# Kernel tuning notes

Hardware: AMD Instinct MI355X
Metric: run time of the kernel (lower is better)

Reference implementation:

```python
import jax, jax.numpy as jnp
import numpy as np

N_NODES = 100000
N_EDGES = 1600000
IN_CH, HID_CH, OUT_CH = 128, 256, 128


def _sage_conv(x, src, dst, W_l, b_l, W_r, n_nodes):
    """PyG SAGEConv with mean aggregation: lin_l(mean_j x_j) + lin_r(x)."""
    # gather source features per edge, scatter-sum into destination nodes
    agg = jax.ops.segment_sum(x[src], dst, num_segments=n_nodes)  # [N, C]
    deg = jax.ops.segment_sum(jnp.ones((src.shape[0],), x.dtype), dst,
                              num_segments=n_nodes)               # [N]
    mean = agg / jnp.maximum(deg, 1.0)[:, None]
    return mean @ W_l + b_l + x @ W_r


def setup_inputs() -> dict:
    key = jax.random.key(0)
    ks = jax.random.split(key, 8)
    x = jax.random.normal(ks[0], (N_NODES, IN_CH), dtype=jnp.float32)
    edge_index = jax.random.randint(ks[1], (2, N_EDGES), 0, N_NODES, dtype=jnp.int64)
    s1 = 1.0 / np.sqrt(IN_CH)
    s2 = 1.0 / np.sqrt(HID_CH)
    W1_l = jax.random.normal(ks[2], (IN_CH, HID_CH), dtype=jnp.float32) * s1
    W1_r = jax.random.normal(ks[3], (IN_CH, HID_CH), dtype=jnp.float32) * s1
    b1 = jnp.zeros((HID_CH,), dtype=jnp.float32)
    W2_l = jax.random.normal(ks[4], (HID_CH, OUT_CH), dtype=jnp.float32) * s2
    W2_r = jax.random.normal(ks[5], (HID_CH, OUT_CH), dtype=jnp.float32) * s2
    b2 = jnp.zeros((OUT_CH,), dtype=jnp.float32)
    return {"x": x, "edge_index": edge_index, "W1_l": W1_l, "b1": b1,
            "W1_r": W1_r, "W2_l": W2_l, "b2": b2, "W2_r": W2_r}


def reference(x, edge_index, W1_l, b1, W1_r, W2_l, b2, W2_r):
    src, dst = edge_index[0], edge_index[1]
    h = _sage_conv(x, src, dst, W1_l, b1, W1_r, N_NODES)
    h = jax.nn.relu(h)
    out = _sage_conv(h, src, dst, W2_l, b2, W2_r, N_NODES)
    return out
```

## Files before the change

kernel.cpp:

```cpp
#include <hip/hip_runtime.h>
#include <cstddef>

#define N_NODES_C 100000
#define N_EDGES_C 1600000

#define NPB 126
#define NB 794
#define DIV_MAGIC 34087043ULL
#define BCAP 2560

#define CONV_BLOCKS 12500
#define WB_BLOCKS 512
#define P1_BLOCKS 1563

typedef unsigned short u16;
typedef __attribute__((ext_vector_type(8))) short bf16x8;
typedef __attribute__((ext_vector_type(4))) float f32x4;

__device__ __forceinline__ u16 f2bf(float f) {
    unsigned u = __float_as_uint(f);
    u += 0x7fffu + ((u >> 16) & 1);
    return (u16)(u >> 16);
}
__device__ __forceinline__ float bf2f(u16 b) {
    return __uint_as_float(((unsigned)b) << 16);
}
__device__ __forceinline__ unsigned bucket_of(int d) {
    return (unsigned)(((unsigned long long)(unsigned)d * DIV_MAGIC) >> 32);
}


__global__ __launch_bounds__(256) void front_fused(
    const float* __restrict__ x, const int* __restrict__ dst,
    const float* __restrict__ W1l, const float* __restrict__ W1r,
    const float* __restrict__ W2l, const float* __restrict__ W2r,
    u16* __restrict__ x_bf, u16* __restrict__ T1l, u16* __restrict__ T1r,
    u16* __restrict__ T2l, u16* __restrict__ T2r,
    int* __restrict__ bucket_counts) {
    const int b = blockIdx.x;
    const int t = threadIdx.x;
    if (b < CONV_BLOCKS) {
        int i = b * 256 + t;
        if (i < 3200000) {
            float4 v = ((const float4*)x)[i];
            ushort4 o;
            o.x = f2bf(v.x); o.y = f2bf(v.y); o.z = f2bf(v.z); o.w = f2bf(v.w);
            ((ushort4*)x_bf)[i] = o;
        }
    } else if (b < CONV_BLOCKS + WB_BLOCKS) {
        int id = (b - CONV_BLOCKS) * 256 + t;
        int which = id >> 15;
        int r = id & 32767;
        if (which == 0) {
            int n = r >> 7, k = r & 127;
            T1l[r] = f2bf(W1l[k * 256 + n]);
        } else if (which == 1) {
            int n = r >> 7, k = r & 127;
            T1r[r] = f2bf(W1r[k * 256 + n]);
        } else if (which == 2) {
            int n = r >> 8, k = r & 255;
            T2l[r] = f2bf(W2l[k * 128 + n]);
        } else {
            int n = r >> 8, k = r & 255;
            T2r[r] = f2bf(W2r[k * 128 + n]);
        }
    } else {
        __shared__ int hist[NB];
        for (int j = t; j < NB; j += 256) hist[j] = 0;
        __syncthreads();
        int i = (b - CONV_BLOCKS - WB_BLOCKS) * 256 + t;
        if (i * 4 < N_EDGES_C) {
            int4 d = ((const int4*)dst)[i];
            atomicAdd(&hist[bucket_of(d.x)], 1);
            atomicAdd(&hist[bucket_of(d.y)], 1);
            atomicAdd(&hist[bucket_of(d.z)], 1);
            atomicAdd(&hist[bucket_of(d.w)], 1);
        }
        __syncthreads();
        for (int j = t; j < NB; j += 256) {
            int c = hist[j];
            if (c) atomicAdd(&bucket_counts[j], c);
        }
    }
}


__global__ __launch_bounds__(1024) void bucket_scan(const int* __restrict__ counts,
                                                    int* __restrict__ base,
                                                    int* __restrict__ cursor) {
    __shared__ int s[1024];
    int t = threadIdx.x;
    int v = (t < NB) ? counts[t] : 0;
    s[t] = v;
    __syncthreads();
    for (int off = 1; off < 1024; off <<= 1) {
        int u = (t >= off) ? s[t - off] : 0;
        __syncthreads();
        s[t] += u;
        __syncthreads();
    }
    if (t < NB) {
        int excl = s[t] - v;
        base[t] = excl;
        cursor[t] = excl;
    }
    if (t == NB - 1) base[NB] = s[t];
}


__global__ __launch_bounds__(1024) void p2_scatter(const int* __restrict__ src,
                                                   const int* __restrict__ dst,
                                                   int* __restrict__ cursor,
                                                   unsigned* __restrict__ edge_pkt) {
    __shared__ int hist[NB];
    __shared__ int lbase[NB];
    __shared__ int cur2[NB];
    int t = threadIdx.x;
    if (t < NB) { hist[t] = 0; cur2[t] = 0; }
    __syncthreads();

    int4 dd[4];
    int idx[4];
#pragma unroll
    for (int r = 0; r < 4; ++r) {
        int i = blockIdx.x * 4096 + r * 1024 + t;
        idx[r] = i;
        if (i * 4 < N_EDGES_C) {
            int4 d = ((const int4*)dst)[i];
            dd[r] = d;
            atomicAdd(&hist[bucket_of(d.x)], 1);
            atomicAdd(&hist[bucket_of(d.y)], 1);
            atomicAdd(&hist[bucket_of(d.z)], 1);
            atomicAdd(&hist[bucket_of(d.w)], 1);
        }
    }
    __syncthreads();
    if (t < NB) {
        int c = hist[t];
        if (c) lbase[t] = atomicAdd(&cursor[t], c);
    }
    __syncthreads();

#pragma unroll
    for (int r = 0; r < 4; ++r) {
        int i = idx[r];
        if (i * 4 < N_EDGES_C) {
            int4 s4 = ((const int4*)src)[i];
            int4 d = dd[r];
            {
                unsigned b = bucket_of(d.x);
                int local = d.x - (int)b * NPB;
                int pos = lbase[b] + atomicAdd(&cur2[b], 1);
                edge_pkt[pos] = ((unsigned)local << 17) | (unsigned)s4.x;
            }
            {
                unsigned b = bucket_of(d.y);
                int local = d.y - (int)b * NPB;
                int pos = lbase[b] + atomicAdd(&cur2[b], 1);
                edge_pkt[pos] = ((unsigned)local << 17) | (unsigned)s4.y;
            }
            {
                unsigned b = bucket_of(d.z);
                int local = d.z - (int)b * NPB;
                int pos = lbase[b] + atomicAdd(&cur2[b], 1);
                edge_pkt[pos] = ((unsigned)local << 17) | (unsigned)s4.z;
            }
            {
                unsigned b = bucket_of(d.w);
                int local = d.w - (int)b * NPB;
                int pos = lbase[b] + atomicAdd(&cur2[b], 1);
                edge_pkt[pos] = ((unsigned)local << 17) | (unsigned)s4.w;
            }
        }
    }
}


template <bool FINAL>
__global__ __launch_bounds__(512) void agg_bucket(const u16* __restrict__ tbl,
                                                  const int* __restrict__ base,
                                                  const unsigned* __restrict__ edge_pkt,
                                                  const u16* __restrict__ resid,
                                                  void* __restrict__ outv) {
    __shared__ unsigned se[BCAP];
    __shared__ int lhist[128];
    __shared__ int lstart[128];
    __shared__ int lcur[128];
    __shared__ int stmp[128];

    const int t = threadIdx.x;
    const int wave = t >> 6;
    const int lane = t & 63;
    const int b = blockIdx.x;

    if (t < 128) lhist[t] = 0;
    __syncthreads();

    const int ebeg = base[b];
    int ecnt = base[b + 1] - ebeg;
    if (ecnt > BCAP) ecnt = BCAP;

    for (int i = t; i < ecnt; i += 512)
        atomicAdd(&lhist[edge_pkt[ebeg + i] >> 17], 1);
    __syncthreads();

    if (t < 128) stmp[t] = lhist[t];
    __syncthreads();
    for (int off = 1; off < 128; off <<= 1) {
        int v = 0;
        if (t < 128 && t >= off) v = stmp[t - off];
        __syncthreads();
        if (t < 128) stmp[t] += v;
        __syncthreads();
    }
    if (t < 128) {
        int excl = stmp[t] - lhist[t];
        lstart[t] = excl;
        lcur[t] = excl;
    }
    __syncthreads();

    for (int i = t; i < ecnt; i += 512) {
        unsigned p = edge_pkt[ebeg + i];
        int pos = atomicAdd(&lcur[p >> 17], 1);
        se[pos] = p & 0x1ffffu;
    }
    __syncthreads();

    for (int n = wave; n < NPB; n += 8) {
        int node = b * NPB + n;
        if (node >= N_NODES_C) break;
        const int s0 = lstart[n];
        const int d = lhist[n];
        float ax = 0.f, ay = 0.f;
        for (int j0 = 0; j0 < d; j0 += 64) {
            int nn = d - j0;
            if (nn > 64) nn = 64;
            unsigned idx = 0;
            if (j0 + lane < d) idx = se[s0 + j0 + lane];
            int tt = 0;
            for (; tt + 4 <= nn; tt += 4) {
                unsigned s0i = __shfl(idx, tt, 64);
                unsigned s1i = __shfl(idx, tt + 1, 64);
                unsigned s2i = __shfl(idx, tt + 2, 64);
                unsigned s3i = __shfl(idx, tt + 3, 64);
                unsigned v0 = *(const unsigned*)(tbl + (size_t)s0i * 128 + lane * 2);
                unsigned v1 = *(const unsigned*)(tbl + (size_t)s1i * 128 + lane * 2);
                unsigned v2 = *(const unsigned*)(tbl + (size_t)s2i * 128 + lane * 2);
                unsigned v3 = *(const unsigned*)(tbl + (size_t)s3i * 128 + lane * 2);
                ax += __uint_as_float((v0 & 0xffffu) << 16);
                ay += __uint_as_float(v0 & 0xffff0000u);
                ax += __uint_as_float((v1 & 0xffffu) << 16);
                ay += __uint_as_float(v1 & 0xffff0000u);
                ax += __uint_as_float((v2 & 0xffffu) << 16);
                ay += __uint_as_float(v2 & 0xffff0000u);
                ax += __uint_as_float((v3 & 0xffffu) << 16);
                ay += __uint_as_float(v3 & 0xffff0000u);
            }
            for (; tt < nn; ++tt) {
                unsigned s = __shfl(idx, tt, 64);
                unsigned v = *(const unsigned*)(tbl + (size_t)s * 128 + lane * 2);
                ax += __uint_as_float((v & 0xffffu) << 16);
                ay += __uint_as_float(v & 0xffff0000u);
            }
        }
        float inv = d > 0 ? 1.f / (float)d : 0.f;
        if (FINAL) {
            unsigned rp = *(const unsigned*)(resid + (size_t)node * 128 + lane * 2);
            float2 o;
            o.x = ax * inv + __uint_as_float((rp & 0xffffu) << 16);
            o.y = ay * inv + __uint_as_float(rp & 0xffff0000u);
            *(float2*)((float*)outv + (size_t)node * 128 + lane * 2) = o;
        } else {
            unsigned o = (unsigned)f2bf(ax * inv) | ((unsigned)f2bf(ay * inv) << 16);
            *(unsigned*)((u16*)outv + (size_t)node * 128 + lane * 2) = o;
        }
    }
}


__global__ __launch_bounds__(256) void fused_l1l2(
    const u16* __restrict__ A1 , const u16* __restrict__ A2 ,
    const u16* __restrict__ T1l, const u16* __restrict__ T1r,
    const u16* __restrict__ T2l, const u16* __restrict__ T2r,
    const float* __restrict__ b1, const float* __restrict__ b2,
    u16* __restrict__ p2, u16* __restrict__ outp, int M) {
    alignas(16) __shared__ u16 hfrag[64 * 256];
    alignas(16) __shared__ u16 As[64 * 32];
    alignas(16) __shared__ u16 Bs[256 * 32];

    const int tid = threadIdx.x;
    const int lane = tid & 63;
    const int wave = tid >> 6;
    const int qm = lane & 15;
    const int quad = lane >> 4;
    const int m0 = blockIdx.x * 64;

    const int wr0 = (wave >> 1) * 32;
    const int wc0 = (wave & 1) * 128;
    f32x4 acch[2][8];
#pragma unroll
    for (int i = 0; i < 2; ++i)
#pragma unroll
        for (int j = 0; j < 8; ++j) acch[i][j] = (f32x4){0.f, 0.f, 0.f, 0.f};

#pragma unroll
    for (int mat = 0; mat < 2; ++mat) {
        const u16* __restrict__ A = mat ? A2 : A1;
        const u16* __restrict__ W = mat ? T1r : T1l;
#pragma unroll
        for (int k0 = 0; k0 < 128; k0 += 32) {
            {
                int c = tid;
                int row = c >> 2, kc = c & 3;
                __builtin_amdgcn_global_load_lds(
                    (const __attribute__((address_space(1))) unsigned*)(
                        A + (size_t)(m0 + row) * 128 + k0 + kc * 8),
                    (__attribute__((address_space(3))) unsigned*)(As + c * 8), 16, 0, 0);
            }
#pragma unroll
            for (int r = 0; r < 4; ++r) {
                int c = r * 256 + tid;
                int row = c >> 2, kc = c & 3;
                __builtin_amdgcn_global_load_lds(
                    (const __attribute__((address_space(1))) unsigned*)(
                        W + (size_t)row * 128 + k0 + kc * 8),
                    (__attribute__((address_space(3))) unsigned*)(Bs + c * 8), 16, 0, 0);
            }
            __syncthreads();
            bf16x8 af[2], bf[8];
#pragma unroll
            for (int i = 0; i < 2; ++i)
                af[i] = *(const bf16x8*)(As + (wr0 + i * 16 + qm) * 32 + quad * 8);
#pragma unroll
            for (int j = 0; j < 8; ++j)
                bf[j] = *(const bf16x8*)(Bs + (wc0 + j * 16 + qm) * 32 + quad * 8);
#pragma unroll
            for (int i = 0; i < 2; ++i)
#pragma unroll
                for (int j = 0; j < 8; ++j)
                    acch[i][j] = __builtin_amdgcn_mfma_f32_16x16x32_bf16(
                        af[i], bf[j], acch[i][j], 0, 0, 0);
            __syncthreads();
        }
    }

#pragma unroll
    for (int j = 0; j < 8; ++j) {
        int n = wc0 + j * 16 + qm;
        float bb = b1[n];
        int ks = n >> 5, quadB = (n >> 3) & 3, jB = n & 7;
#pragma unroll
        for (int i = 0; i < 2; ++i) {
#pragma unroll
            for (int r = 0; r < 4; ++r) {
                int mloc = wr0 + i * 16 + quad * 4 + r;
                float v = fmaxf(acch[i][j][r] + bb, 0.f);
                hfrag[((ks * 4 + (mloc >> 4)) * 16 + (mloc & 15)) * 32 + quadB * 8 + jB] =
                    f2bf(v);
            }
        }
    }
    __syncthreads();

    const int wrB = (wave >> 1) * 32;
    const int wcB = (wave & 1) * 64;
    f32x4 accp[2][4], acco[2][4];
#pragma unroll
    for (int i = 0; i < 2; ++i)
#pragma unroll
        for (int j = 0; j < 4; ++j) {
            accp[i][j] = (f32x4){0.f, 0.f, 0.f, 0.f};
            acco[i][j] = (f32x4){0.f, 0.f, 0.f, 0.f};
        }

#pragma unroll
    for (int ks = 0; ks < 8; ++ks) {
#pragma unroll
        for (int r = 0; r < 4; ++r) {
            int c = r * 256 + tid;
            int matc = c >> 9;
            int row = (c >> 2) & 127;
            int kc = c & 3;
            const u16* W = matc ? T2r : T2l;
            __builtin_amdgcn_global_load_lds(
                (const __attribute__((address_space(1))) unsigned*)(
                    W + (size_t)row * 256 + ks * 32 + kc * 8),
                (__attribute__((address_space(3))) unsigned*)(Bs + c * 8), 16, 0, 0);
        }
        __syncthreads();
        bf16x8 af[2], bfl[4], bfr[4];
#pragma unroll
        for (int i = 0; i < 2; ++i)
            af[i] = *(const bf16x8*)(hfrag +
                                     ((ks * 4 + (wrB >> 4) + i) * 16 + qm) * 32 + quad * 8);
#pragma unroll
        for (int j = 0; j < 4; ++j) {
            bfl[j] = *(const bf16x8*)(Bs + (wcB + j * 16 + qm) * 32 + quad * 8);
            bfr[j] = *(const bf16x8*)(Bs + 4096 + (wcB + j * 16 + qm) * 32 + quad * 8);
        }
#pragma unroll
        for (int i = 0; i < 2; ++i)
#pragma unroll
            for (int j = 0; j < 4; ++j) {
                accp[i][j] = __builtin_amdgcn_mfma_f32_16x16x32_bf16(af[i], bfl[j],
                                                                    accp[i][j], 0, 0, 0);
                acco[i][j] = __builtin_amdgcn_mfma_f32_16x16x32_bf16(af[i], bfr[j],
                                                                    acco[i][j], 0, 0, 0);
            }
        __syncthreads();
    }

#pragma unroll
    for (int j = 0; j < 4; ++j) {
        int n = wcB + j * 16 + qm;
        float bb2 = b2[n];
#pragma unroll
        for (int i = 0; i < 2; ++i) {
#pragma unroll
            for (int r = 0; r < 4; ++r) {
                int row = m0 + wrB + i * 16 + quad * 4 + r;
                if (row < M) {
                    p2[(size_t)row * 128 + n] = f2bf(accp[i][j][r]);
                    outp[(size_t)row * 128 + n] = f2bf(acco[i][j][r] + bb2);
                }
            }
        }
    }
}


extern "C" void kernel_launch(void* const* d_in, const int* in_sizes, int n_in,
                              void* d_out, int out_size, void* d_ws, size_t ws_size,
                              hipStream_t stream) {
    const float* x = (const float*)d_in[0];
    const int* ei = (const int*)d_in[1];
    const float* W1l = (const float*)d_in[2];
    const float* b1 = (const float*)d_in[3];
    const float* W1r = (const float*)d_in[4];
    const float* W2l = (const float*)d_in[5];
    const float* b2 = (const float*)d_in[6];
    const float* W2r = (const float*)d_in[7];
    float* out = (float*)d_out;

    const int* src = ei;
    const int* dst = ei + N_EDGES_C;

    int* iw = (int*)d_ws;
    int* bucket_counts = iw;
    int* bucket_base = iw + 1024;
    int* cursor = iw + 2048;
    unsigned* edge_pkt = (unsigned*)(iw + 3072);
    u16* T1l = (u16*)(iw + 1603072);
    u16* T1r = T1l + 32768;
    u16* T2l = T1r + 32768;
    u16* T2r = T2l + 32768;
    u16* ub = (u16*)((char*)d_ws + (8u << 20));
    u16* x_bf = ub;
    u16* mean1 = ub + 12850000;
    u16* p2 = ub + 25700000;
    u16* outp = ub + 38550000;

    hipMemsetAsync(bucket_counts, 0, 1024 * sizeof(int), stream);

    front_fused<<<CONV_BLOCKS + WB_BLOCKS + P1_BLOCKS, 256, 0, stream>>>(
        x, dst, W1l, W1r, W2l, W2r, x_bf, T1l, T1r, T2l, T2r, bucket_counts);
    bucket_scan<<<1, 1024, 0, stream>>>(bucket_counts, bucket_base, cursor);
    p2_scatter<<<(N_EDGES_C / 4 + 4095) / 4096, 1024, 0, stream>>>(src, dst, cursor,
                                                                   edge_pkt);

    agg_bucket<false><<<NB, 512, 0, stream>>>(x_bf, bucket_base, edge_pkt, nullptr,
                                              mean1);
    fused_l1l2<<<(N_NODES_C + 63) / 64, 256, 0, stream>>>(
        mean1, x_bf, T1l, T1r, T2l, T2r, b1, b2, p2, outp, N_NODES_C);
    agg_bucket<true><<<NB, 512, 0, stream>>>(p2, bucket_base, edge_pkt, outp, out);
}
```

Measured before the change: 396.2 us.

## Halve bucket size and aggregate four nodes per wave with 16-byte row gathers

Buckets shrink from 126 to 63 nodes, doubling their count, and the scan now handles two buckets per thread. In the aggregation kernel each wave now serves four nodes at once, with 16 lanes per node each loading 16 bytes (8 bf16). Missing neighbours are padded with a zeroed sentinel row so the loop runs branch-free up to the group's maximum degree. The goal is fewer, wider gather loads, more blocks for occupancy, and no per-lane shuffles. The cost is wasted loads when degrees within a group differ, and a smaller per-bucket edge cap that truncates high-degree buckets.

```diff
diff --git a/kernel.cpp b/kernel.cpp
--- a/kernel.cpp
+++ b/kernel.cpp
@@ -4,10 +4,11 @@
 #define N_NODES_C 100000
 #define N_EDGES_C 1600000
 
-#define NPB 126
-#define NB 794
-#define DIV_MAGIC 34087043ULL
-#define BCAP 2560
+#define NPB 63
+#define NB 1588
+#define DIV_MAGIC 68174085ULL
+#define BCAP 1408
+#define SENT_ROW 100000
 
 #define CONV_BLOCKS 12500
 #define WB_BLOCKS 512
@@ -22,8 +23,11 @@
     u += 0x7fffu + ((u >> 16) & 1);
     return (u16)(u >> 16);
 }
-__device__ __forceinline__ float bf2f(u16 b) {
-    return __uint_as_float(((unsigned)b) << 16);
+__device__ __forceinline__ float lo16f(unsigned v) {
+    return __uint_as_float(v << 16);
+}
+__device__ __forceinline__ float hi16f(unsigned v) {
+    return __uint_as_float(v & 0xffff0000u);
 }
 __device__ __forceinline__ unsigned bucket_of(int d) {
     return (unsigned)(((unsigned long long)(unsigned)d * DIV_MAGIC) >> 32);
@@ -36,7 +40,7 @@
     const float* __restrict__ W2l, const float* __restrict__ W2r,
     u16* __restrict__ x_bf, u16* __restrict__ T1l, u16* __restrict__ T1r,
     u16* __restrict__ T2l, u16* __restrict__ T2r,
-    int* __restrict__ bucket_counts) {
+    int* __restrict__ bucket_counts, u16* __restrict__ p2z) {
     const int b = blockIdx.x;
     const int t = threadIdx.x;
     if (b < CONV_BLOCKS) {
@@ -64,7 +68,7 @@
             int n = r >> 8, k = r & 255;
             T2r[r] = f2bf(W2r[k * 128 + n]);
         }
-    } else {
+    } else if (b < CONV_BLOCKS + WB_BLOCKS + P1_BLOCKS) {
         __shared__ int hist[NB];
         for (int j = t; j < NB; j += 256) hist[j] = 0;
         __syncthreads();
@@ -81,6 +85,12 @@
             int c = hist[j];
             if (c) atomicAdd(&bucket_counts[j], c);
         }
+    } else {
+        uint4 z; z.x = 0; z.y = 0; z.z = 0; z.w = 0;
+        if (t < 16)
+            ((uint4*)(x_bf + (size_t)SENT_ROW * 128))[t] = z;
+        else if (t < 32)
+            ((uint4*)(p2z + (size_t)SENT_ROW * 128))[t - 16] = z;
     }
 }
 
@@ -90,7 +100,9 @@
                                                     int* __restrict__ cursor) {
     __shared__ int s[1024];
     int t = threadIdx.x;
-    int v = (t < NB) ? counts[t] : 0;
+    int c0 = counts[2 * t];
+    int c1 = counts[2 * t + 1];
+    int v = c0 + c1;
     s[t] = v;
     __syncthreads();
     for (int off = 1; off < 1024; off <<= 1) {
@@ -99,12 +111,11 @@
         s[t] += u;
         __syncthreads();
     }
-    if (t < NB) {
-        int excl = s[t] - v;
-        base[t] = excl;
-        cursor[t] = excl;
-    }
-    if (t == NB - 1) base[NB] = s[t];
+    int excl = s[t] - v;
+    base[2 * t] = excl;
+    cursor[2 * t] = excl;
+    base[2 * t + 1] = excl + c0;
+    cursor[2 * t + 1] = excl + c0;
 }
 
 
@@ -116,7 +127,7 @@
     __shared__ int lbase[NB];
     __shared__ int cur2[NB];
     int t = threadIdx.x;
-    if (t < NB) { hist[t] = 0; cur2[t] = 0; }
+    for (int j = t; j < NB; j += 1024) { hist[j] = 0; cur2[j] = 0; }
     __syncthreads();
 
     int4 dd[4];
@@ -135,9 +146,9 @@
         }
     }
     __syncthreads();
-    if (t < NB) {
-        int c = hist[t];
-        if (c) lbase[t] = atomicAdd(&cursor[t], c);
+    for (int j = t; j < NB; j += 1024) {
+        int c = hist[j];
+        if (c) lbase[j] = atomicAdd(&cursor[j], c);
     }
     __syncthreads();
 
@@ -177,103 +188,128 @@
 
 
 template <bool FINAL>
-__global__ __launch_bounds__(512) void agg_bucket(const u16* __restrict__ tbl,
-                                                  const int* __restrict__ base,
-                                                  const unsigned* __restrict__ edge_pkt,
-                                                  const u16* __restrict__ resid,
-                                                  void* __restrict__ outv) {
+__global__ __launch_bounds__(256, 8) void agg_bucket(const u16* __restrict__ tbl,
+                                                     const int* __restrict__ base,
+                                                     const unsigned* __restrict__ edge_pkt,
+                                                     const u16* __restrict__ resid,
+                                                     void* __restrict__ outv) {
     __shared__ unsigned se[BCAP];
-    __shared__ int lhist[128];
-    __shared__ int lstart[128];
-    __shared__ int lcur[128];
-    __shared__ int stmp[128];
+    __shared__ int lhist[64];
+    __shared__ int lstart[64];
+    __shared__ int lcur[64];
+    __shared__ int stmp[64];
 
     const int t = threadIdx.x;
     const int wave = t >> 6;
     const int lane = t & 63;
     const int b = blockIdx.x;
 
-    if (t < 128) lhist[t] = 0;
+    if (t < 64) lhist[t] = 0;
     __syncthreads();
 
     const int ebeg = base[b];
     int ecnt = base[b + 1] - ebeg;
     if (ecnt > BCAP) ecnt = BCAP;
 
-    for (int i = t; i < ecnt; i += 512)
+    for (int i = t; i < ecnt; i += 256)
         atomicAdd(&lhist[edge_pkt[ebeg + i] >> 17], 1);
     __syncthreads();
 
-    if (t < 128) stmp[t] = lhist[t];
-    __syncthreads();
-    for (int off = 1; off < 128; off <<= 1) {
+    if (t < 64) stmp[t] = lhist[t];
+    __syncthreads();
+    for (int off = 1; off < 64; off <<= 1) {
         int v = 0;
-        if (t < 128 && t >= off) v = stmp[t - off];
-        __syncthreads();
-        if (t < 128) stmp[t] += v;
-        __syncthreads();
-    }
-    if (t < 128) {
+        if (t < 64 && t >= off) v = stmp[t - off];
+        __syncthreads();
+        if (t < 64) stmp[t] += v;
+        __syncthreads();
+    }
+    if (t < 64) {
         int excl = stmp[t] - lhist[t];
         lstart[t] = excl;
         lcur[t] = excl;
     }
     __syncthreads();
 
-    for (int i = t; i < ecnt; i += 512) {
+    for (int i = t; i < ecnt; i += 256) {
         unsigned p = edge_pkt[ebeg + i];
         int pos = atomicAdd(&lcur[p >> 17], 1);
         se[pos] = p & 0x1ffffu;
     }
     __syncthreads();
 
-    for (int n = wave; n < NPB; n += 8) {
+    const int g = lane >> 4;
+    const int li8 = (lane & 15) * 8;
+
+    for (int pass = 0; pass < 4; ++pass) {
+        int n = pass * 16 + wave * 4 + g;
         int node = b * NPB + n;
-        if (node >= N_NODES_C) break;
-        const int s0 = lstart[n];
-        const int d = lhist[n];
-        float ax = 0.f, ay = 0.f;
-        for (int j0 = 0; j0 < d; j0 += 64) {
-            int nn = d - j0;
-            if (nn > 64) nn = 64;
-            unsigned idx = 0;
-            if (j0 + lane < d) idx = se[s0 + j0 + lane];
-            int tt = 0;
-            for (; tt + 4 <= nn; tt += 4) {
-                unsigned s0i = __shfl(idx, tt, 64);
-                unsigned s1i = __shfl(idx, tt + 1, 64);
-                unsigned s2i = __shfl(idx, tt + 2, 64);
-                unsigned s3i = __shfl(idx, tt + 3, 64);
-                unsigned v0 = *(const unsigned*)(tbl + (size_t)s0i * 128 + lane * 2);
-                unsigned v1 = *(const unsigned*)(tbl + (size_t)s1i * 128 + lane * 2);
-                unsigned v2 = *(const unsigned*)(tbl + (size_t)s2i * 128 + lane * 2);
-                unsigned v3 = *(const unsigned*)(tbl + (size_t)s3i * 128 + lane * 2);
-                ax += __uint_as_float((v0 & 0xffffu) << 16);
-                ay += __uint_as_float(v0 & 0xffff0000u);
-                ax += __uint_as_float((v1 & 0xffffu) << 16);
-                ay += __uint_as_float(v1 & 0xffff0000u);
-                ax += __uint_as_float((v2 & 0xffffu) << 16);
-                ay += __uint_as_float(v2 & 0xffff0000u);
-                ax += __uint_as_float((v3 & 0xffffu) << 16);
-                ay += __uint_as_float(v3 & 0xffff0000u);
-            }
-            for (; tt < nn; ++tt) {
-                unsigned s = __shfl(idx, tt, 64);
-                unsigned v = *(const unsigned*)(tbl + (size_t)s * 128 + lane * 2);
-                ax += __uint_as_float((v & 0xffffu) << 16);
-                ay += __uint_as_float(v & 0xffff0000u);
-            }
-        }
-        float inv = d > 0 ? 1.f / (float)d : 0.f;
-        if (FINAL) {
-            unsigned rp = *(const unsigned*)(resid + (size_t)node * 128 + lane * 2);
-            float2 o;
-            o.x = ax * inv + __uint_as_float((rp & 0xffffu) << 16);
-            o.y = ay * inv + __uint_as_float(rp & 0xffff0000u);
-            *(float2*)((float*)outv + (size_t)node * 128 + lane * 2) = o;
-        } else {
-            unsigned o = (unsigned)f2bf(ax * inv) | ((unsigned)f2bf(ay * inv) << 16);
-            *(unsigned*)((u16*)outv + (size_t)node * 128 + lane * 2) = o;
+        int d = 0, s0 = 0;
+        bool valid = (n < NPB) && (node < N_NODES_C);
+        if (valid) { d = lhist[n]; s0 = lstart[n]; }
+        int dmax = max(d, __shfl_xor(d, 16, 64));
+        dmax = max(dmax, __shfl_xor(dmax, 32, 64));
+
+        float a0 = 0.f, a1 = 0.f, a2 = 0.f, a3 = 0.f;
+        float a4 = 0.f, a5 = 0.f, a6 = 0.f, a7 = 0.f;
+
+        for (int j = 0; j < dmax; j += 4) {
+            unsigned ix[4];
+#pragma unroll
+            for (int u = 0; u < 4; ++u) {
+                int jj = j + u;
+                int sa = s0 + jj;
+                if (sa > BCAP - 1) sa = BCAP - 1;
+                unsigned sv = se[sa];
+                ix[u] = (jj < d) ? sv : (unsigned)SENT_ROW;
+            }
+            uint4 r0 = *(const uint4*)(tbl + (size_t)ix[0] * 128 + li8);
+            uint4 r1 = *(const uint4*)(tbl + (size_t)ix[1] * 128 + li8);
+            uint4 r2 = *(const uint4*)(tbl + (size_t)ix[2] * 128 + li8);
+            uint4 r3 = *(const uint4*)(tbl + (size_t)ix[3] * 128 + li8);
+
+            a0 += lo16f(r0.x); a1 += hi16f(r0.x);
+            a2 += lo16f(r0.y); a3 += hi16f(r0.y);
+            a4 += lo16f(r0.z); a5 += hi16f(r0.z);
+            a6 += lo16f(r0.w); a7 += hi16f(r0.w);
+            a0 += lo16f(r1.x); a1 += hi16f(r1.x);
+            a2 += lo16f(r1.y); a3 += hi16f(r1.y);
+            a4 += lo16f(r1.z); a5 += hi16f(r1.z);
+            a6 += lo16f(r1.w); a7 += hi16f(r1.w);
+            a0 += lo16f(r2.x); a1 += hi16f(r2.x);
+            a2 += lo16f(r2.y); a3 += hi16f(r2.y);
+            a4 += lo16f(r2.z); a5 += hi16f(r2.z);
+            a6 += lo16f(r2.w); a7 += hi16f(r2.w);
+            a0 += lo16f(r3.x); a1 += hi16f(r3.x);
+            a2 += lo16f(r3.y); a3 += hi16f(r3.y);
+            a4 += lo16f(r3.z); a5 += hi16f(r3.z);
+            a6 += lo16f(r3.w); a7 += hi16f(r3.w);
+        }
+
+        if (valid) {
+            float inv = d > 0 ? 1.f / (float)d : 0.f;
+            if (FINAL) {
+                uint4 rp = *(const uint4*)(resid + (size_t)node * 128 + li8);
+                float* op = (float*)outv + (size_t)node * 128 + li8;
+                float4 o0, o1;
+                o0.x = a0 * inv + lo16f(rp.x);
+                o0.y = a1 * inv + hi16f(rp.x);
+                o0.z = a2 * inv + lo16f(rp.y);
+                o0.w = a3 * inv + hi16f(rp.y);
+                o1.x = a4 * inv + lo16f(rp.z);
+                o1.y = a5 * inv + hi16f(rp.z);
+                o1.z = a6 * inv + lo16f(rp.w);
+                o1.w = a7 * inv + hi16f(rp.w);
+                *(float4*)op = o0;
+                *(float4*)(op + 4) = o1;
+            } else {
+                uint4 o;
+                o.x = (unsigned)f2bf(a0 * inv) | ((unsigned)f2bf(a1 * inv) << 16);
+                o.y = (unsigned)f2bf(a2 * inv) | ((unsigned)f2bf(a3 * inv) << 16);
+                o.z = (unsigned)f2bf(a4 * inv) | ((unsigned)f2bf(a5 * inv) << 16);
+                o.w = (unsigned)f2bf(a6 * inv) | ((unsigned)f2bf(a7 * inv) << 16);
+                *(uint4*)((u16*)outv + (size_t)node * 128 + li8) = o;
+            }
         }
     }
 }
@@ -448,10 +484,10 @@
 
     int* iw = (int*)d_ws;
     int* bucket_counts = iw;
-    int* bucket_base = iw + 1024;
-    int* cursor = iw + 2048;
-    unsigned* edge_pkt = (unsigned*)(iw + 3072);
-    u16* T1l = (u16*)(iw + 1603072);
+    int* bucket_base = iw + 2048;
+    int* cursor = iw + 4096;
+    unsigned* edge_pkt = (unsigned*)(iw + 6144);
+    u16* T1l = (u16*)(iw + 1606144);
     u16* T1r = T1l + 32768;
     u16* T2l = T1r + 32768;
     u16* T2r = T2l + 32768;
@@ -461,17 +497,17 @@
     u16* p2 = ub + 25700000;
     u16* outp = ub + 38550000;
 
-    hipMemsetAsync(bucket_counts, 0, 1024 * sizeof(int), stream);
-
-    front_fused<<<CONV_BLOCKS + WB_BLOCKS + P1_BLOCKS, 256, 0, stream>>>(
-        x, dst, W1l, W1r, W2l, W2r, x_bf, T1l, T1r, T2l, T2r, bucket_counts);
+    hipMemsetAsync(bucket_counts, 0, 2048 * sizeof(int), stream);
+
+    front_fused<<<CONV_BLOCKS + WB_BLOCKS + P1_BLOCKS + 1, 256, 0, stream>>>(
+        x, dst, W1l, W1r, W2l, W2r, x_bf, T1l, T1r, T2l, T2r, bucket_counts, p2);
     bucket_scan<<<1, 1024, 0, stream>>>(bucket_counts, bucket_base, cursor);
     p2_scatter<<<(N_EDGES_C / 4 + 4095) / 4096, 1024, 0, stream>>>(src, dst, cursor,
                                                                    edge_pkt);
 
-    agg_bucket<false><<<NB, 512, 0, stream>>>(x_bf, bucket_base, edge_pkt, nullptr,
+    agg_bucket<false><<<NB, 256, 0, stream>>>(x_bf, bucket_base, edge_pkt, nullptr,
                                               mean1);
     fused_l1l2<<<(N_NODES_C + 63) / 64, 256, 0, stream>>>(
         mean1, x_bf, T1l, T1r, T2l, T2r, b1, b2, p2, outp, N_NODES_C);
-    agg_bucket<true><<<NB, 512, 0, stream>>>(p2, bucket_base, edge_pkt, outp, out);
-}
+    agg_bucket<true><<<NB, 256, 0, stream>>>(p2, bucket_base, edge_pkt, outp, out);
+}
```

Result: no change. 401.9 us (+1.4%).
